# Kernel tuning notes

Measured on AMD Instinct MI355X. Metric: run time of the kernel, lower is better.

## Reference

```python
import jax, jax.numpy as jnp
import numpy as np


def setup_inputs() -> dict:
    key = jax.random.key(0)
    k1, k2 = jax.random.split(key)
    B, N, M, D = 4, 1024, 1024, 64
    traj1 = jax.random.normal(k1, (B, N, D), dtype=jnp.float32)
    traj2 = jax.random.normal(k2, (B, M, D), dtype=jnp.float32)
    return {"traj1": traj1, "traj2": traj2}


def reference(traj1, traj2):
    # Pairwise squared Euclidean distances: [B, N, M]
    # Faithful to sum((traj1[:, :, None] - traj2[:, None, :])**2, -1)
    diff = traj1[:, :, None, :] - traj2[:, None, :, :]  # [B, N, M, D]
    return jnp.sum(jnp.square(diff), axis=-1)
```

## Files before the change

### kernel.cpp

```cpp
#include <hip/hip_runtime.h>


#define B_ 4
#define N_ 1024
#define M_ 1024
#define D_ 64
#define BN 128
#define BM 128

__device__ __forceinline__ int swz(int k) { return ((k >> 2) & 7) << 2; }

__global__ __launch_bounds__(256, 1)
void dist2_kernel(const float* __restrict__ A, const float* __restrict__ Bm,
                  float* __restrict__ out) {
  __shared__ float As[D_][BN];
  __shared__ float Bs[D_][BM];
  __shared__ float naS[BN];
  __shared__ float nbS[BM];

  const int tid = threadIdx.x;
  const int b  = blockIdx.z;
  const int n0 = blockIdx.y * BN;
  const int m0 = blockIdx.x * BM;

  const float* Ap = A  + ((size_t)b * N_ + n0) * D_;
  const float* Bp = Bm + ((size_t)b * M_ + m0) * D_;

  #pragma unroll
  for (int i = 0; i < (BN * (D_ / 4)) / 256; ++i) {
    int f  = tid + i * 256;
    int n  = f >> 4;
    int k4 = f & 15;
    float4 v = *reinterpret_cast<const float4*>(Ap + n * D_ + k4 * 4);
    int k  = k4 << 2;
    int nn = n ^ swz(k);
    As[k + 0][nn] = v.x; As[k + 1][nn] = v.y;
    As[k + 2][nn] = v.z; As[k + 3][nn] = v.w;
  }
  #pragma unroll
  for (int i = 0; i < (BM * (D_ / 4)) / 256; ++i) {
    int f  = tid + i * 256;
    int m  = f >> 4;
    int k4 = f & 15;
    float4 v = *reinterpret_cast<const float4*>(Bp + m * D_ + k4 * 4);
    int k  = k4 << 2;
    int mm = m ^ swz(k);
    Bs[k + 0][mm] = v.x; Bs[k + 1][mm] = v.y;
    Bs[k + 2][mm] = v.z; Bs[k + 3][mm] = v.w;
  }
  __syncthreads();

  if (tid < BN) {
    float s = 0.f;
    #pragma unroll 8
    for (int k = 0; k < D_; ++k) {
      float v = As[k][tid ^ swz(k)];
      s = fmaf(v, v, s);
    }
    naS[tid] = s;
  } else {
    int m = tid - BN;
    float s = 0.f;
    #pragma unroll 8
    for (int k = 0; k < D_; ++k) {
      float v = Bs[k][m ^ swz(k)];
      s = fmaf(v, v, s);
    }
    nbS[m] = s;
  }
  __syncthreads();

  const int ty = tid >> 4;
  const int tx = tid & 15;

  float acc[8][8];
  #pragma unroll
  for (int i = 0; i < 8; ++i)
    #pragma unroll
    for (int j = 0; j < 8; ++j) acc[i][j] = 0.f;

  #pragma unroll 4
  for (int k = 0; k < D_; ++k) {
    const int sw = swz(k);
    float4 a0 = *reinterpret_cast<const float4*>(&As[k][(ty * 4) ^ sw]);
    float4 a1 = *reinterpret_cast<const float4*>(&As[k][(64 + ty * 4) ^ sw]);
    float4 b0 = *reinterpret_cast<const float4*>(&Bs[k][(tx * 4) ^ sw]);
    float4 b1 = *reinterpret_cast<const float4*>(&Bs[k][(64 + tx * 4) ^ sw]);
    float av[8] = {a0.x, a0.y, a0.z, a0.w, a1.x, a1.y, a1.z, a1.w};
    float bv[8] = {b0.x, b0.y, b0.z, b0.w, b1.x, b1.y, b1.z, b1.w};
    #pragma unroll
    for (int i = 0; i < 8; ++i)
      #pragma unroll
      for (int j = 0; j < 8; ++j)
        acc[i][j] = fmaf(av[i], bv[j], acc[i][j]);
  }

  float4 na0 = *reinterpret_cast<const float4*>(&naS[ty * 4]);
  float4 na1 = *reinterpret_cast<const float4*>(&naS[64 + ty * 4]);
  float4 nb0 = *reinterpret_cast<const float4*>(&nbS[tx * 4]);
  float4 nb1 = *reinterpret_cast<const float4*>(&nbS[64 + tx * 4]);
  float nav[8] = {na0.x, na0.y, na0.z, na0.w, na1.x, na1.y, na1.z, na1.w};
  float nbv[8] = {nb0.x, nb0.y, nb0.z, nb0.w, nb1.x, nb1.y, nb1.z, nb1.w};

  #pragma unroll
  for (int i = 0; i < 8; ++i) {
    int row = n0 + ((i < 4) ? (ty * 4 + i) : (64 + ty * 4 + (i - 4)));
    float* orow = out + ((size_t)b * N_ + row) * M_ + m0;
    float4 r0, r1;
    r0.x = fmaf(-2.f, acc[i][0], nav[i] + nbv[0]);
    r0.y = fmaf(-2.f, acc[i][1], nav[i] + nbv[1]);
    r0.z = fmaf(-2.f, acc[i][2], nav[i] + nbv[2]);
    r0.w = fmaf(-2.f, acc[i][3], nav[i] + nbv[3]);
    r1.x = fmaf(-2.f, acc[i][4], nav[i] + nbv[4]);
    r1.y = fmaf(-2.f, acc[i][5], nav[i] + nbv[5]);
    r1.z = fmaf(-2.f, acc[i][6], nav[i] + nbv[6]);
    r1.w = fmaf(-2.f, acc[i][7], nav[i] + nbv[7]);
    *reinterpret_cast<float4*>(orow + tx * 4)      = r0;
    *reinterpret_cast<float4*>(orow + 64 + tx * 4) = r1;
  }
}

extern "C" void kernel_launch(void* const* d_in, const int* in_sizes, int n_in,
                              void* d_out, int out_size, void* d_ws, size_t ws_size,
                              hipStream_t stream) {
  const float* A  = (const float*)d_in[0];
  const float* Bm = (const float*)d_in[1];
  float* out = (float*)d_out;
  dim3 grid(M_ / BM, N_ / BN, B_);
  dist2_kernel<<<grid, dim3(256), 0, stream>>>(A, Bm, out);
}
```

Before: 17.42 us.

## Replace FP32 FMA tile with fp16 MFMA loaded directly from global

Rewrites the cross-term computation to use 16x16x32 fp16 MFMA instructions, converting fp32 inputs to fp16 in registers. Operands now come straight from global memory rather than through the swizzled shared-memory tiles, and each block uses 512 threads arranged as 8 waves. Norms are still computed in fp32 from global. The aim is to cut the FMA cost of the FP32 outer product. The price is a precision loss: fp16 rounding of the inputs feeds the -2ab term, which may break accuracy tolerance. Output stores are now scalar, strided per lane.

```diff
diff --git a/kernel.cpp b/kernel.cpp
--- a/kernel.cpp
+++ b/kernel.cpp
@@ -8,13 +8,29 @@
 #define BN 128
 #define BM 128
 
-__device__ __forceinline__ int swz(int k) { return ((k >> 2) & 7) << 2; }
+typedef __attribute__((ext_vector_type(8))) __fp16 f16x8;
+typedef __attribute__((ext_vector_type(2))) __fp16 f16x2;
+typedef __attribute__((ext_vector_type(4))) float f32x4;
 
-__global__ __launch_bounds__(256, 1)
-void dist2_kernel(const float* __restrict__ A, const float* __restrict__ Bm,
-                  float* __restrict__ out) {
-  __shared__ float As[D_][BN];
-  __shared__ float Bs[D_][BM];
+union F16x8 {
+  f16x8 v;
+  f16x2 h[4];
+};
+
+__device__ __forceinline__ f16x8 load_frag8(const float* __restrict__ p) {
+  float4 v0 = *reinterpret_cast<const float4*>(p);
+  float4 v1 = *reinterpret_cast<const float4*>(p + 4);
+  F16x8 r;
+  r.h[0] = __builtin_amdgcn_cvt_pkrtz(v0.x, v0.y);
+  r.h[1] = __builtin_amdgcn_cvt_pkrtz(v0.z, v0.w);
+  r.h[2] = __builtin_amdgcn_cvt_pkrtz(v1.x, v1.y);
+  r.h[3] = __builtin_amdgcn_cvt_pkrtz(v1.z, v1.w);
+  return r.v;
+}
+
+__global__ __launch_bounds__(512, 4)
+void dist2_mfma(const float* __restrict__ A, const float* __restrict__ Bm,
+                float* __restrict__ out) {
   __shared__ float naS[BN];
   __shared__ float nbS[BM];
 
@@ -23,100 +39,74 @@
   const int n0 = blockIdx.y * BN;
   const int m0 = blockIdx.x * BM;
 
-  const float* Ap = A  + ((size_t)b * N_ + n0) * D_;
-  const float* Bp = Bm + ((size_t)b * M_ + m0) * D_;
+  const float* Ab = A  + (size_t)b * N_ * D_;
+  const float* Bb = Bm + (size_t)b * M_ * D_;
+
+  if (tid < BN + BM) {
+    const float* p = (tid < BN) ? (Ab + (size_t)(n0 + tid) * D_)
+                                : (Bb + (size_t)(m0 + tid - BN) * D_);
+    float s = 0.f;
+    #pragma unroll
+    for (int k4 = 0; k4 < D_ / 4; ++k4) {
+      float4 v = *reinterpret_cast<const float4*>(p + k4 * 4);
+      s = fmaf(v.x, v.x, s);
+      s = fmaf(v.y, v.y, s);
+      s = fmaf(v.z, v.z, s);
+      s = fmaf(v.w, v.w, s);
+    }
+    if (tid < BN) naS[tid] = s; else nbS[tid - BN] = s;
+  }
+
+  const int wid  = tid >> 6;
+  const int lane = tid & 63;
+  const int wrow = wid >> 2;
+  const int wcol = wid & 3;
+  const int lr    = lane & 15;
+  const int kbase = (lane >> 4) * 8;
+
+  const float* Arow = Ab + (size_t)(n0 + wrow * 64 + lr) * D_;
+  const float* Brow = Bb + (size_t)(m0 + wcol * 32 + lr) * D_;
+
+  f32x4 acc[4][2];
+  #pragma unroll
+  for (int i = 0; i < 4; ++i)
+    #pragma unroll
+    for (int j = 0; j < 2; ++j) acc[i][j] = (f32x4){0.f, 0.f, 0.f, 0.f};
 
   #pragma unroll
-  for (int i = 0; i < (BN * (D_ / 4)) / 256; ++i) {
-    int f  = tid + i * 256;
-    int n  = f >> 4;
-    int k4 = f & 15;
-    float4 v = *reinterpret_cast<const float4*>(Ap + n * D_ + k4 * 4);
-    int k  = k4 << 2;
-    int nn = n ^ swz(k);
-    As[k + 0][nn] = v.x; As[k + 1][nn] = v.y;
-    As[k + 2][nn] = v.z; As[k + 3][nn] = v.w;
+  for (int ks = 0; ks < 2; ++ks) {
+    const int k = ks * 32 + kbase;
+    f16x8 af[4], bf[2];
+    #pragma unroll
+    for (int i = 0; i < 4; ++i) af[i] = load_frag8(Arow + (size_t)i * 16 * D_ + k);
+    #pragma unroll
+    for (int j = 0; j < 2; ++j) bf[j] = load_frag8(Brow + (size_t)j * 16 * D_ + k);
+    #pragma unroll
+    for (int i = 0; i < 4; ++i)
+      #pragma unroll
+      for (int j = 0; j < 2; ++j)
+        acc[i][j] = __builtin_amdgcn_mfma_f32_16x16x32_f16(af[i], bf[j], acc[i][j], 0, 0, 0);
   }
-  #pragma unroll
-  for (int i = 0; i < (BM * (D_ / 4)) / 256; ++i) {
-    int f  = tid + i * 256;
-    int m  = f >> 4;
-    int k4 = f & 15;
-    float4 v = *reinterpret_cast<const float4*>(Bp + m * D_ + k4 * 4);
-    int k  = k4 << 2;
-    int mm = m ^ swz(k);
-    Bs[k + 0][mm] = v.x; Bs[k + 1][mm] = v.y;
-    Bs[k + 2][mm] = v.z; Bs[k + 3][mm] = v.w;
-  }
+
   __syncthreads();
 
-  if (tid < BN) {
-    float s = 0.f;
-    #pragma unroll 8
-    for (int k = 0; k < D_; ++k) {
-      float v = As[k][tid ^ swz(k)];
-      s = fmaf(v, v, s);
-    }
-    naS[tid] = s;
-  } else {
-    int m = tid - BN;
-    float s = 0.f;
-    #pragma unroll 8
-    for (int k = 0; k < D_; ++k) {
-      float v = Bs[k][m ^ swz(k)];
-      s = fmaf(v, v, s);
-    }
-    nbS[m] = s;
-  }
-  __syncthreads();
-
-  const int ty = tid >> 4;
-  const int tx = tid & 15;
-
-  float acc[8][8];
-  #pragma unroll
-  for (int i = 0; i < 8; ++i)
-    #pragma unroll
-    for (int j = 0; j < 8; ++j) acc[i][j] = 0.f;
-
-  #pragma unroll 4
-  for (int k = 0; k < D_; ++k) {
-    const int sw = swz(k);
-    float4 a0 = *reinterpret_cast<const float4*>(&As[k][(ty * 4) ^ sw]);
-    float4 a1 = *reinterpret_cast<const float4*>(&As[k][(64 + ty * 4) ^ sw]);
-    float4 b0 = *reinterpret_cast<const float4*>(&Bs[k][(tx * 4) ^ sw]);
-    float4 b1 = *reinterpret_cast<const float4*>(&Bs[k][(64 + tx * 4) ^ sw]);
-    float av[8] = {a0.x, a0.y, a0.z, a0.w, a1.x, a1.y, a1.z, a1.w};
-    float bv[8] = {b0.x, b0.y, b0.z, b0.w, b1.x, b1.y, b1.z, b1.w};
-    #pragma unroll
-    for (int i = 0; i < 8; ++i)
-      #pragma unroll
-      for (int j = 0; j < 8; ++j)
-        acc[i][j] = fmaf(av[i], bv[j], acc[i][j]);
-  }
-
-  float4 na0 = *reinterpret_cast<const float4*>(&naS[ty * 4]);
-  float4 na1 = *reinterpret_cast<const float4*>(&naS[64 + ty * 4]);
-  float4 nb0 = *reinterpret_cast<const float4*>(&nbS[tx * 4]);
-  float4 nb1 = *reinterpret_cast<const float4*>(&nbS[64 + tx * 4]);
-  float nav[8] = {na0.x, na0.y, na0.z, na0.w, na1.x, na1.y, na1.z, na1.w};
-  float nbv[8] = {nb0.x, nb0.y, nb0.z, nb0.w, nb1.x, nb1.y, nb1.z, nb1.w};
+  const int colA  = lane & 15;
+  const int rbase = (lane >> 4) * 4;
 
   #pragma unroll
-  for (int i = 0; i < 8; ++i) {
-    int row = n0 + ((i < 4) ? (ty * 4 + i) : (64 + ty * 4 + (i - 4)));
-    float* orow = out + ((size_t)b * N_ + row) * M_ + m0;
-    float4 r0, r1;
-    r0.x = fmaf(-2.f, acc[i][0], nav[i] + nbv[0]);
-    r0.y = fmaf(-2.f, acc[i][1], nav[i] + nbv[1]);
-    r0.z = fmaf(-2.f, acc[i][2], nav[i] + nbv[2]);
-    r0.w = fmaf(-2.f, acc[i][3], nav[i] + nbv[3]);
-    r1.x = fmaf(-2.f, acc[i][4], nav[i] + nbv[4]);
-    r1.y = fmaf(-2.f, acc[i][5], nav[i] + nbv[5]);
-    r1.z = fmaf(-2.f, acc[i][6], nav[i] + nbv[6]);
-    r1.w = fmaf(-2.f, acc[i][7], nav[i] + nbv[7]);
-    *reinterpret_cast<float4*>(orow + tx * 4)      = r0;
-    *reinterpret_cast<float4*>(orow + 64 + tx * 4) = r1;
+  for (int i = 0; i < 4; ++i) {
+    #pragma unroll
+    for (int j = 0; j < 2; ++j) {
+      const int   col = wcol * 32 + j * 16 + colA;
+      const float nb  = nbS[col];
+      #pragma unroll
+      for (int q = 0; q < 4; ++q) {
+        const int row = wrow * 64 + i * 16 + rbase + q;
+        const float na = naS[row];
+        out[((size_t)b * N_ + n0 + row) * M_ + m0 + col] =
+            fmaf(-2.f, acc[i][j][q], na + nb);
+      }
+    }
   }
 }
 
@@ -127,5 +117,5 @@
   const float* Bm = (const float*)d_in[1];
   float* out = (float*)d_out;
   dim3 grid(M_ / BM, N_ / BN, B_);
-  dist2_kernel<<<grid, dim3(256), 0, stream>>>(A, Bm, out);
+  dist2_mfma<<<grid, dim3(512), 0, stream>>>(A, Bm, out);
 }
```

New measurement: 16.89 us. 3.1% less time.
